# Kernel optimization log

Measured on AMD Instinct MI355X. Metric: run time of the kernel, lower is better.

## Reference

```python
import jax, jax.numpy as jnp
import numpy as np

N_NODES = 468  # MediaPipe face-mesh landmark count


def build_edges(n):
    # static edge structure from create_face_graph: i <-> j for j in i+1..min(i+10, n)
    src, dst = [], []
    for i in range(n):
        for j in range(i + 1, min(i + 10, n)):
            src += [i, j]
            dst += [j, i]
    # PyG GCNConv adds self-loops before normalization
    src = np.asarray(src + list(range(n)), dtype=np.int32)
    dst = np.asarray(dst + list(range(n)), dtype=np.int32)
    deg = np.bincount(dst, minlength=n).astype(np.float32)
    dinv = 1.0 / np.sqrt(deg)
    norm = (dinv[src] * dinv[dst]).astype(np.float32)
    return jnp.asarray(src), jnp.asarray(dst), jnp.asarray(norm)


def gcn_conv(x, W, b, src, dst, norm):
    # x: [B, N, d_in] -> [B, N, d_out]; GCNConv: transform then normalized scatter-add
    h = x @ W                                   # [B, N, d_out]
    msg = h[:, src, :] * norm[None, :, None]    # gather along node dim: [B, E, d_out]
    agg = jnp.zeros_like(h).at[:, dst, :].add(msg)
    return agg + b


def setup_inputs() -> dict:
    key = jax.random.key(0)
    ks = jax.random.split(key, 13)
    s = 0.05
    inp = {
        'landmarks': jax.random.normal(ks[0], (128, N_NODES * 3), dtype=jnp.float32),
        'W_enc': jax.random.normal(ks[1], (3, 64), dtype=jnp.float32) * s,
        'b_enc': jnp.zeros((64,), dtype=jnp.float32),
        'W1': jax.random.normal(ks[2], (64, 128), dtype=jnp.float32) * s,
        'b1': jnp.zeros((128,), dtype=jnp.float32),
        'W2': jax.random.normal(ks[3], (128, 256), dtype=jnp.float32) * s,
        'b2': jnp.zeros((256,), dtype=jnp.float32),
        'W3': jax.random.normal(ks[4], (256, 128), dtype=jnp.float32) * s,
        'b3': jnp.zeros((128,), dtype=jnp.float32),
        'W_fus': jax.random.normal(ks[5], (128, 512), dtype=jnp.float32) * s,
        'b_fus': jnp.zeros((512,), dtype=jnp.float32),
        'W_cls': jax.random.normal(ks[6], (512, 2), dtype=jnp.float32) * s,
        'b_cls': jnp.zeros((2,), dtype=jnp.float32),
    }
    return inp


def reference(landmarks, W_enc, b_enc, W1, b1, W2, b2, W3, b3, W_fus, b_fus, W_cls, b_cls):
    B = landmarks.shape[0]
    n = landmarks.shape[1] // 3
    src, dst, norm = build_edges(n)
    x = landmarks.reshape(B, n, 3) @ W_enc + b_enc            # node encoder [B,N,64]
    x = jax.nn.relu(gcn_conv(x, W1, b1, src, dst, norm))      # [B,N,128]
    x = jax.nn.relu(gcn_conv(x, W2, b2, src, dst, norm))      # [B,N,256]
    x = jax.nn.relu(gcn_conv(x, W3, b3, src, dst, norm))      # [B,N,128]
    graph_features = jnp.mean(x, axis=1)                      # global mean pool [B,128]
    features = jax.nn.relu(graph_features @ W_fus + b_fus)    # fusion (dropout=eval) [B,512]
    output = features @ W_cls + b_cls                         # classifier [B,2]
    return output, features, graph_features
```

## Files before the change

kernel.cpp:

```cpp
#include <hip/hip_runtime.h>
#include <hip/hip_bf16.h>

typedef __bf16 bf16x8 __attribute__((ext_vector_type(8)));
typedef float  f32x4  __attribute__((ext_vector_type(4)));
typedef unsigned short ushort_t;

#define NN 468

#define W1H 0
#define W1L 8192
#define W2H 16384
#define W2L 49152
#define W3H 81920
#define W3L 114688

#define L_X0   0
#define L_X1   0
#define L_X2   0
#define R1     43296
#define L_DTAB 76064
#define L_POOL 76544

#define MFMA3(d, ah, al, wh, wl)                                        \
    d = __builtin_amdgcn_mfma_f32_16x16x32_bf16(ah, wh, d, 0, 0, 0);    \
    d = __builtin_amdgcn_mfma_f32_16x16x32_bf16(ah, wl, d, 0, 0, 0);    \
    d = __builtin_amdgcn_mfma_f32_16x16x32_bf16(al, wh, d, 0, 0, 0);

__device__ __forceinline__ void pack_split4(const float* y,
                                            ushort_t* hdst, ushort_t* ldst) {
    ushort_t h[4], l[4];
    #pragma unroll
    for (int j = 0; j < 4; ++j) {
        __hip_bfloat16 hb = __float2bfloat16(y[j]);
        float hf = __bfloat162float(hb);
        __hip_bfloat16 lb = __float2bfloat16(y[j] - hf);
        h[j] = *(ushort_t*)&hb; l[j] = *(ushort_t*)&lb;
    }
    uint2 hv = make_uint2((unsigned)h[0] | ((unsigned)h[1] << 16),
                          (unsigned)h[2] | ((unsigned)h[3] << 16));
    uint2 lv = make_uint2((unsigned)l[0] | ((unsigned)l[1] << 16),
                          (unsigned)l[2] | ((unsigned)l[3] << 16));
    *(uint2*)hdst = hv;
    *(uint2*)ldst = lv;
}

__device__ __forceinline__ int frag_off(int r, int k, int K16) {
    return (r >> 4) * K16 + (k >> 5) * 512 + ((k >> 3) & 3) * 128
         + (r & 15) * 8 + (k & 7);
}

__device__ __forceinline__ int ywoff(int r, int k4, int K16) {
    int q = (k4 >> 3) & 3;
    int u = q * 16 + (((r & 15) ^ (q << 1)) & 15);
    return (r >> 4) * K16 + (k4 >> 5) * 512 + u * 8 + (k4 & 7);
}

__global__ __launch_bounds__(512, 4) void fused(
    const float* __restrict__ Lm, const ushort_t* __restrict__ wext,
    const float* __restrict__ We, const float* __restrict__ be,
    const float* __restrict__ b1, const float* __restrict__ b2,
    const float* __restrict__ b3, float* __restrict__ partial)
{
    __shared__ __align__(16) char lds[77056];
    float*    X0   = (float*)(lds + L_X0);
    float*    X1   = (float*)(lds + L_X1);
    float*    X2   = (float*)(lds + L_X2);
    float*    lmst = (float*)(lds + R1);
    ushort_t* Y1h  = (ushort_t*)(lds + R1);  ushort_t* Y1l = Y1h + 7168;
    ushort_t* Y2h  = (ushort_t*)(lds + R1);  ushort_t* Y2l = Y2h + 6144;
    ushort_t* Y3h  = (ushort_t*)(lds + R1);  ushort_t* Y3l = Y3h + 8192;
    float*    dtab = (float*)(lds + L_DTAB);
    float*    pool = (float*)(lds + L_POOL);

    const int tid  = threadIdx.x;
    const int lane = tid & 63;
    const int wave = tid >> 6;
    const int wm = wave & 1, wn = wave >> 1;
    const int l15 = lane & 15, lg = lane >> 4;
    const int lswz = (lane & 48) + (((lane & 15) ^ ((lane >> 4) << 1)) & 15);
    const int rt = blockIdx.x, b = blockIdx.y;
    const int r0 = rt * 64;

    if (tid < 118) {
        int ri = r0 - 27 + tid;
        float dv = 0.f;
        if (ri >= 0 && ri < NN) {
            int lo = ri - 9; if (lo < 0) lo = 0;
            int hi = ri + 9; if (hi > NN - 1) hi = NN - 1;
            dv = 1.0f / sqrtf((float)(hi - lo + 1));
        }
        dtab[tid] = dv;
    }
    if (tid < 354) {
        int g = (r0 - 27) * 3 + tid;
        lmst[tid] = (g >= 0 && g < NN * 3) ? Lm[(size_t)b * (NN * 3) + g] : 0.f;
    }
    if (tid < 128) pool[tid] = 0.f;
    __syncthreads();

    {
        const int c = tid & 63;
        const float w0 = We[c], w1 = We[64 + c], w2 = We[128 + c], bk = be[c];
        for (int l0 = tid >> 6; l0 < 118; l0 += 8) {
            float x = bk + lmst[l0*3]*w0 + lmst[l0*3+1]*w1 + lmst[l0*3+2]*w2;
            X0[l0 * 68 + c] = x * dtab[l0];
        }
    }
    __syncthreads();

    {
        const int c4 = (tid & 15) << 2;
        const int base = (tid >> 4) * 4;
        if (base < 100) {
            f32x4 ws = {};
            #pragma unroll
            for (int d = 0; d < 19; ++d)
                ws += *(const f32x4*)(X0 + (base + d) * 68 + c4);
            #pragma unroll
            for (int rr = 0; rr < 4; ++rr) {
                int row = base + rr;
                if (rr) ws += *(const f32x4*)(X0 + (row + 18) * 68 + c4)
                            - *(const f32x4*)(X0 + (row - 1)  * 68 + c4);
                float dv = dtab[row + 9];
                float y4[4] = {ws[0]*dv, ws[1]*dv, ws[2]*dv, ws[3]*dv};
                int off = ywoff(row, c4, 1024);
                pack_split4(y4, Y1h + off, Y1l + off);
            }
        } else if (base < 112) {
            float z4[4] = {0.f, 0.f, 0.f, 0.f};
            #pragma unroll
            for (int rr = 0; rr < 4; ++rr) {
                int row = base + rr;
                if (row < 112) {
                    int off = ywoff(row, c4, 1024);
                    pack_split4(z4, Y1h + off, Y1l + off);
                }
            }
        }
    }
    __syncthreads();

    f32x4 acc1[4][2] = {};
    __builtin_amdgcn_s_setprio(1);
    #pragma unroll
    for (int kt = 0; kt < 2; ++kt) {
        bf16x8 a[4][2];
        #pragma unroll
        for (int mt = 0; mt < 4; ++mt) {
            int t = wm*4 + mt; if (t > 6) t = 6;
            int off = t * 1024 + kt * 512 + lswz * 8;
            a[mt][0] = *(const bf16x8*)(Y1h + off);
            a[mt][1] = *(const bf16x8*)(Y1l + off);
        }
        #pragma unroll
        for (int nt = 0; nt < 2; ++nt) {
            int woff = (nt*4 + wn) * 1024 + kt * 512 + lane * 8;
            bf16x8 wh = *(const bf16x8*)(wext + W1H + woff);
            bf16x8 wl = *(const bf16x8*)(wext + W1L + woff);
            #pragma unroll
            for (int mt = 0; mt < 4; ++mt) {
                MFMA3(acc1[mt][nt], a[mt][0], a[mt][1], wh, wl);
            }
        }
    }
    __builtin_amdgcn_s_setprio(0);

    f32x4 acc2[3][4] = {};
    #pragma unroll
    for (int kc = 0; kc < 2; ++kc) {
        if (kc == 1) {
            __builtin_amdgcn_s_setprio(1);
            #pragma unroll
            for (int kt = 0; kt < 2; ++kt) {
                bf16x8 a[3][2];
                #pragma unroll
                for (int mt = 0; mt < 3; ++mt) {
                    int off = (wm*3 + mt) * 1024 + kt * 512 + lswz * 8;
                    a[mt][0] = *(const bf16x8*)(Y2h + off);
                    a[mt][1] = *(const bf16x8*)(Y2l + off);
                }
                #pragma unroll
                for (int nt = 0; nt < 4; ++nt) {
                    int woff = (nt*4 + wn) * 2048 + (0*2 + kt) * 512 + lane * 8;
                    bf16x8 wh = *(const bf16x8*)(wext + W2H + woff);
                    bf16x8 wl = *(const bf16x8*)(wext + W2L + woff);
                    #pragma unroll
                    for (int mt = 0; mt < 3; ++mt) {
                        MFMA3(acc2[mt][nt], a[mt][0], a[mt][1], wh, wl);
                    }
                }
            }
            __builtin_amdgcn_s_setprio(0);
        }
        #pragma unroll
        for (int mt = 0; mt < 4; ++mt) {
            int t = wm*4 + mt; if (t > 6) t = 6;
            int gcol = (kc*4 + wn)*16 + l15;
            int cl   = wn*16 + l15;
            float bv = b1[gcol];
            #pragma unroll
            for (int r = 0; r < 4; ++r) {
                int lr1 = t*16 + lg*4 + r;
                if (lr1 < 100)
                    X1[lr1*68 + cl] =
                        dtab[lr1 + 9] * fmaxf(acc1[mt][kc][r] + bv, 0.f);
            }
        }
        __syncthreads();

        {
            const int c4   = (tid & 15) << 2;
            const int base = (tid >> 4) * 3;
            f32x4 ws = {};
            if (base < 82) {
                #pragma unroll
                for (int d = 0; d < 19; ++d)
                    ws += *(const f32x4*)(X1 + (base + d) * 68 + c4);
            }
            #pragma unroll
            for (int rr = 0; rr < 3; ++rr) {
                int row = base + rr;
                if (row < 96) {
                    float y4[4] = {0.f, 0.f, 0.f, 0.f};
                    if (row < 82) {
                        if (rr) ws += *(const f32x4*)(X1 + (row + 18) * 68 + c4)
                                    - *(const f32x4*)(X1 + (row - 1)  * 68 + c4);
                        float dv = dtab[row + 18];
                        y4[0] = ws[0]*dv; y4[1] = ws[1]*dv;
                        y4[2] = ws[2]*dv; y4[3] = ws[3]*dv;
                    }
                    int off = ywoff(row, c4, 1024);
                    pack_split4(y4, Y2h + off, Y2l + off);
                }
            }
        }
        __syncthreads();
    }

    __builtin_amdgcn_s_setprio(1);
    #pragma unroll
    for (int kt = 0; kt < 2; ++kt) {
        bf16x8 a[3][2];
        #pragma unroll
        for (int mt = 0; mt < 3; ++mt) {
            int off = (wm*3 + mt) * 1024 + kt * 512 + lswz * 8;
            a[mt][0] = *(const bf16x8*)(Y2h + off);
            a[mt][1] = *(const bf16x8*)(Y2l + off);
        }
        #pragma unroll
        for (int nt = 0; nt < 4; ++nt) {
            int woff = (nt*4 + wn) * 2048 + (1*2 + kt) * 512 + lane * 8;
            bf16x8 wh = *(const bf16x8*)(wext + W2H + woff);
            bf16x8 wl = *(const bf16x8*)(wext + W2L + woff);
            #pragma unroll
            for (int mt = 0; mt < 3; ++mt) {
                MFMA3(acc2[mt][nt], a[mt][0], a[mt][1], wh, wl);
            }
        }
    }
    __builtin_amdgcn_s_setprio(0);

    f32x4 acc3[2][2] = {};
    #pragma unroll
    for (int nc = 0; nc < 2; ++nc) {
        if (nc == 1) {
            __builtin_amdgcn_s_setprio(1);
            #pragma unroll
            for (int kt = 0; kt < 4; ++kt) {
                bf16x8 a0[2], a1[2];
                #pragma unroll
                for (int mt = 0; mt < 2; ++mt) {
                    int aoff = (wm*2 + mt) * 2048 + kt * 512 + lswz * 8;
                    a0[mt] = *(const bf16x8*)(Y3h + aoff);
                    a1[mt] = *(const bf16x8*)(Y3l + aoff);
                }
                #pragma unroll
                for (int nt = 0; nt < 2; ++nt) {
                    int woff = (nt*4 + wn) * 4096 + (0*4 + kt) * 512 + lane * 8;
                    bf16x8 wh = *(const bf16x8*)(wext + W3H + woff);
                    bf16x8 wl = *(const bf16x8*)(wext + W3L + woff);
                    #pragma unroll
                    for (int mt = 0; mt < 2; ++mt) {
                        MFMA3(acc3[mt][nt], a0[mt], a1[mt], wh, wl);
                    }
                }
            }
            __builtin_amdgcn_s_setprio(0);
        }
        #pragma unroll
        for (int mt = 0; mt < 3; ++mt)
        #pragma unroll
        for (int q = 0; q < 2; ++q) {
            int gcol = ((nc*2 + q)*4 + wn)*16 + l15;
            int cl   = (q*4 + wn)*16 + l15;
            float bv = b2[gcol];
            #pragma unroll
            for (int r = 0; r < 4; ++r) {
                int lr2 = (wm*3 + mt)*16 + lg*4 + r;
                if (lr2 < 82)
                    X2[lr2*132 + cl] =
                        dtab[lr2 + 18] * fmaxf(acc2[mt][nc*2 + q][r] + bv, 0.f);
            }
        }
        __syncthreads();

        {
            const int c4   = (tid & 31) << 2;
            const int base = (tid >> 5) * 4;
            f32x4 ws = {};
            #pragma unroll
            for (int d = 0; d < 19; ++d)
                ws += *(const f32x4*)(X2 + (base + d) * 132 + c4);
            #pragma unroll
            for (int rr = 0; rr < 4; ++rr) {
                int row = base + rr;
                if (rr) ws += *(const f32x4*)(X2 + (row + 18) * 132 + c4)
                            - *(const f32x4*)(X2 + (row - 1)  * 132 + c4);
                float dv = dtab[row + 27];
                float y4[4] = {ws[0]*dv, ws[1]*dv, ws[2]*dv, ws[3]*dv};
                int off = ywoff(row, c4, 2048);
                pack_split4(y4, Y3h + off, Y3l + off);
            }
        }
        __syncthreads();
    }

    __builtin_amdgcn_s_setprio(1);
    #pragma unroll
    for (int kt = 0; kt < 4; ++kt) {
        bf16x8 a0[2], a1[2];
        #pragma unroll
        for (int mt = 0; mt < 2; ++mt) {
            int aoff = (wm*2 + mt) * 2048 + kt * 512 + lswz * 8;
            a0[mt] = *(const bf16x8*)(Y3h + aoff);
            a1[mt] = *(const bf16x8*)(Y3l + aoff);
        }
        #pragma unroll
        for (int nt = 0; nt < 2; ++nt) {
            int woff = (nt*4 + wn) * 4096 + (1*4 + kt) * 512 + lane * 8;
            bf16x8 wh = *(const bf16x8*)(wext + W3H + woff);
            bf16x8 wl = *(const bf16x8*)(wext + W3L + woff);
            #pragma unroll
            for (int mt = 0; mt < 2; ++mt) {
                MFMA3(acc3[mt][nt], a0[mt], a1[mt], wh, wl);
            }
        }
    }
    __builtin_amdgcn_s_setprio(0);

    #pragma unroll
    for (int nt = 0; nt < 2; ++nt) {
        int g_t = nt*4 + wn;
        float bv = b3[g_t*16 + l15];
        float cs = 0.f;
        #pragma unroll
        for (int mt = 0; mt < 2; ++mt)
        #pragma unroll
        for (int r = 0; r < 4; ++r) {
            int gr = r0 + (wm*2 + mt)*16 + lg*4 + r;
            if (gr < NN) cs += fmaxf(acc3[mt][nt][r] + bv, 0.f);
        }
        cs += __shfl_xor(cs, 16);
        cs += __shfl_xor(cs, 32);
        if (lane < 16) atomicAdd(&pool[g_t*16 + lane], cs);
    }
    __syncthreads();
    if (tid < 128) partial[((size_t)b * 8 + rt) * 128 + tid] = pool[tid];
}

__global__ __launch_bounds__(256) void wconv(
    const float* __restrict__ W1, const float* __restrict__ W2,
    const float* __restrict__ W3, ushort_t* __restrict__ wext)
{
    int i = blockIdx.x * 256 + threadIdx.x;
    float w; int off_h, off_l, idx;
    if (i < 8192) {
        int k = i >> 7, n = i & 127;
        w = W1[i]; idx = frag_off(n, k, 1024);  off_h = W1H; off_l = W1L;
    } else if (i < 40960) {
        int j = i - 8192;
        int k = j >> 8, n = j & 255;
        w = W2[j]; idx = frag_off(n, k, 2048);  off_h = W2H; off_l = W2L;
    } else if (i < 73728) {
        int j = i - 40960;
        int k = j >> 7, n = j & 127;
        w = W3[j]; idx = frag_off(n, k, 4096);  off_h = W3H; off_l = W3L;
    } else return;
    __hip_bfloat16 hb = __float2bfloat16(w);
    float hf = __bfloat162float(hb);
    __hip_bfloat16 lb = __float2bfloat16(w - hf);
    wext[off_h + idx] = *(ushort_t*)&hb;
    wext[off_l + idx] = *(ushort_t*)&lb;
}

__global__ __launch_bounds__(512) void head_kernel(
    const float* __restrict__ partial, const float* __restrict__ Wf,
    const float* __restrict__ bf, const float* __restrict__ Wc,
    const float* __restrict__ bc, float* __restrict__ dout)
{
    __shared__ float gfs[128];
    __shared__ float feats[512];
    int b = blockIdx.x, t = threadIdx.x;
    if (t < 128) {
        const float* p = partial + (size_t)b * (8 * 128);
        float s = 0.f;
        #pragma unroll
        for (int tt = 0; tt < 8; ++tt) s += p[tt * 128 + t];
        s *= (1.0f / 468.0f);
        gfs[t] = s;
        dout[65792 + b * 128 + t] = s;
    }
    __syncthreads();
    float a = bf[t];
    for (int k = 0; k < 128; ++k) a += gfs[k] * Wf[k * 512 + t];
    a = fmaxf(a, 0.f);
    dout[256 + b * 512 + t] = a;
    feats[t] = a;
    __syncthreads();
    if (t < 64) {
        float s0 = 0.f, s1 = 0.f;
        for (int c = t; c < 512; c += 64) {
            float f = feats[c];
            s0 += f * Wc[c * 2 + 0];
            s1 += f * Wc[c * 2 + 1];
        }
        #pragma unroll
        for (int off = 32; off; off >>= 1) {
            s0 += __shfl_down(s0, off);
            s1 += __shfl_down(s1, off);
        }
        if (t == 0) {
            dout[b * 2 + 0] = s0 + bc[0];
            dout[b * 2 + 1] = s1 + bc[1];
        }
    }
}

extern "C" void kernel_launch(void* const* d_in, const int* in_sizes, int n_in,
                              void* d_out, int out_size, void* d_ws, size_t ws_size,
                              hipStream_t stream)
{
    const float* landmarks = (const float*)d_in[0];
    const float* W_enc     = (const float*)d_in[1];
    const float* b_enc     = (const float*)d_in[2];
    const float* W1        = (const float*)d_in[3];
    const float* b1        = (const float*)d_in[4];
    const float* W2        = (const float*)d_in[5];
    const float* b2        = (const float*)d_in[6];
    const float* W3        = (const float*)d_in[7];
    const float* b3        = (const float*)d_in[8];
    const float* W_fus     = (const float*)d_in[9];
    const float* b_fus     = (const float*)d_in[10];
    const float* W_cls     = (const float*)d_in[11];
    const float* b_cls     = (const float*)d_in[12];
    float* out = (float*)d_out;

    char* ws = (char*)d_ws;
    ushort_t* wext = (ushort_t*)(ws + 0);
    float* partial = (float*)(ws + 294912);

    wconv<<<288, 256, 0, stream>>>(W1, W2, W3, wext);
    fused<<<dim3(8, 128), 512, 0, stream>>>(
        landmarks, wext, W_enc, b_enc, b1, b2, b3, partial);
    head_kernel<<<128, 512, 0, stream>>>(partial, W_fus, b_fus, W_cls, b_cls, out);
}
```

Measured before the change: 69.59 us.

## Store full Y2 in separate LDS region and run layer-2 GEMM after both chunks

Gives the layer-2 aggregated input Y2 a full 128-column buffer at its own LDS offset instead of reusing one half-size region per column chunk. The two K-chunks of the layer-2 GEMM, previously interleaved with the aggregation passes, now run as one 4-step K loop after both chunks are written. LDS is re-laid out with new offsets and grows slightly, and a barrier is added before layer 3. This lowers register pressure during aggregation and gives one longer MFMA loop, but loses the overlap of chunk-0 MFMAs with chunk-1 aggregation and may reduce occupancy.

```diff
diff --git a/kernel.cpp b/kernel.cpp
--- a/kernel.cpp
+++ b/kernel.cpp
@@ -14,12 +14,12 @@
 #define W3H 81920
 #define W3L 114688
 
-#define L_X0   0
-#define L_X1   0
-#define L_X2   0
-#define R1     43296
-#define L_DTAB 76064
-#define L_POOL 76544
+#define L_Y1   32096
+#define L_Y2   27200
+#define L_Y3   43296
+#define L_LM   76352
+#define L_DTAB 77768
+#define L_POOL 78240
 
 #define MFMA3(d, ah, al, wh, wl)                                        \
     d = __builtin_amdgcn_mfma_f32_16x16x32_bf16(ah, wh, d, 0, 0, 0);    \
@@ -61,14 +61,12 @@
     const float* __restrict__ b1, const float* __restrict__ b2,
     const float* __restrict__ b3, float* __restrict__ partial)
 {
-    __shared__ __align__(16) char lds[77056];
-    float*    X0   = (float*)(lds + L_X0);
-    float*    X1   = (float*)(lds + L_X1);
-    float*    X2   = (float*)(lds + L_X2);
-    float*    lmst = (float*)(lds + R1);
-    ushort_t* Y1h  = (ushort_t*)(lds + R1);  ushort_t* Y1l = Y1h + 7168;
-    ushort_t* Y2h  = (ushort_t*)(lds + R1);  ushort_t* Y2l = Y2h + 6144;
-    ushort_t* Y3h  = (ushort_t*)(lds + R1);  ushort_t* Y3l = Y3h + 8192;
+    __shared__ __align__(16) char lds[78752];
+    float*    X    = (float*)(lds);
+    ushort_t* Y1h  = (ushort_t*)(lds + L_Y1);  ushort_t* Y1l = Y1h + 7168;
+    ushort_t* Y2h  = (ushort_t*)(lds + L_Y2);  ushort_t* Y2l = Y2h + 12288;
+    ushort_t* Y3h  = (ushort_t*)(lds + L_Y3);  ushort_t* Y3l = Y3h + 8192;
+    float*    lmst = (float*)(lds + L_LM);
     float*    dtab = (float*)(lds + L_DTAB);
     float*    pool = (float*)(lds + L_POOL);
 
@@ -103,7 +101,7 @@
         const float w0 = We[c], w1 = We[64 + c], w2 = We[128 + c], bk = be[c];
         for (int l0 = tid >> 6; l0 < 118; l0 += 8) {
             float x = bk + lmst[l0*3]*w0 + lmst[l0*3+1]*w1 + lmst[l0*3+2]*w2;
-            X0[l0 * 68 + c] = x * dtab[l0];
+            X[l0 * 68 + c] = x * dtab[l0];
         }
     }
     __syncthreads();
@@ -115,12 +113,12 @@
             f32x4 ws = {};
             #pragma unroll
             for (int d = 0; d < 19; ++d)
-                ws += *(const f32x4*)(X0 + (base + d) * 68 + c4);
+                ws += *(const f32x4*)(X + (base + d) * 68 + c4);
             #pragma unroll
             for (int rr = 0; rr < 4; ++rr) {
                 int row = base + rr;
-                if (rr) ws += *(const f32x4*)(X0 + (row + 18) * 68 + c4)
-                            - *(const f32x4*)(X0 + (row - 1)  * 68 + c4);
+                if (rr) ws += *(const f32x4*)(X + (row + 18) * 68 + c4)
+                            - *(const f32x4*)(X + (row - 1)  * 68 + c4);
                 float dv = dtab[row + 9];
                 float y4[4] = {ws[0]*dv, ws[1]*dv, ws[2]*dv, ws[3]*dv};
                 int off = ywoff(row, c4, 1024);
@@ -165,33 +163,8 @@
     }
     __builtin_amdgcn_s_setprio(0);
 
-    f32x4 acc2[3][4] = {};
     #pragma unroll
     for (int kc = 0; kc < 2; ++kc) {
-        if (kc == 1) {
-            __builtin_amdgcn_s_setprio(1);
-            #pragma unroll
-            for (int kt = 0; kt < 2; ++kt) {
-                bf16x8 a[3][2];
-                #pragma unroll
-                for (int mt = 0; mt < 3; ++mt) {
-                    int off = (wm*3 + mt) * 1024 + kt * 512 + lswz * 8;
-                    a[mt][0] = *(const bf16x8*)(Y2h + off);
-                    a[mt][1] = *(const bf16x8*)(Y2l + off);
-                }
-                #pragma unroll
-                for (int nt = 0; nt < 4; ++nt) {
-                    int woff = (nt*4 + wn) * 2048 + (0*2 + kt) * 512 + lane * 8;
-                    bf16x8 wh = *(const bf16x8*)(wext + W2H + woff);
-                    bf16x8 wl = *(const bf16x8*)(wext + W2L + woff);
-                    #pragma unroll
-                    for (int mt = 0; mt < 3; ++mt) {
-                        MFMA3(acc2[mt][nt], a[mt][0], a[mt][1], wh, wl);
-                    }
-                }
-            }
-            __builtin_amdgcn_s_setprio(0);
-        }
         #pragma unroll
         for (int mt = 0; mt < 4; ++mt) {
             int t = wm*4 + mt; if (t > 6) t = 6;
@@ -202,7 +175,7 @@
             for (int r = 0; r < 4; ++r) {
                 int lr1 = t*16 + lg*4 + r;
                 if (lr1 < 100)
-                    X1[lr1*68 + cl] =
+                    X[lr1*68 + cl] =
                         dtab[lr1 + 9] * fmaxf(acc1[mt][kc][r] + bv, 0.f);
             }
         }
@@ -215,7 +188,7 @@
             if (base < 82) {
                 #pragma unroll
                 for (int d = 0; d < 19; ++d)
-                    ws += *(const f32x4*)(X1 + (base + d) * 68 + c4);
+                    ws += *(const f32x4*)(X + (base + d) * 68 + c4);
             }
             #pragma unroll
             for (int rr = 0; rr < 3; ++rr) {
@@ -223,13 +196,13 @@
                 if (row < 96) {
                     float y4[4] = {0.f, 0.f, 0.f, 0.f};
                     if (row < 82) {
-                        if (rr) ws += *(const f32x4*)(X1 + (row + 18) * 68 + c4)
-                                    - *(const f32x4*)(X1 + (row - 1)  * 68 + c4);
+                        if (rr) ws += *(const f32x4*)(X + (row + 18) * 68 + c4)
+                                    - *(const f32x4*)(X + (row - 1)  * 68 + c4);
                         float dv = dtab[row + 18];
                         y4[0] = ws[0]*dv; y4[1] = ws[1]*dv;
                         y4[2] = ws[2]*dv; y4[3] = ws[3]*dv;
                     }
-                    int off = ywoff(row, c4, 1024);
+                    int off = ywoff(row, kc*64 + c4, 2048);
                     pack_split4(y4, Y2h + off, Y2l + off);
                 }
             }
@@ -237,19 +210,20 @@
         __syncthreads();
     }
 
+    f32x4 acc2[3][4] = {};
     __builtin_amdgcn_s_setprio(1);
     #pragma unroll
-    for (int kt = 0; kt < 2; ++kt) {
+    for (int kt = 0; kt < 4; ++kt) {
         bf16x8 a[3][2];
         #pragma unroll
         for (int mt = 0; mt < 3; ++mt) {
-            int off = (wm*3 + mt) * 1024 + kt * 512 + lswz * 8;
+            int off = (wm*3 + mt) * 2048 + kt * 512 + lswz * 8;
             a[mt][0] = *(const bf16x8*)(Y2h + off);
             a[mt][1] = *(const bf16x8*)(Y2l + off);
         }
         #pragma unroll
         for (int nt = 0; nt < 4; ++nt) {
-            int woff = (nt*4 + wn) * 2048 + (1*2 + kt) * 512 + lane * 8;
+            int woff = (nt*4 + wn) * 2048 + kt * 512 + lane * 8;
             bf16x8 wh = *(const bf16x8*)(wext + W2H + woff);
             bf16x8 wl = *(const bf16x8*)(wext + W2L + woff);
             #pragma unroll
@@ -259,6 +233,7 @@
         }
     }
     __builtin_amdgcn_s_setprio(0);
+    __syncthreads();
 
     f32x4 acc3[2][2] = {};
     #pragma unroll
@@ -298,7 +273,7 @@
             for (int r = 0; r < 4; ++r) {
                 int lr2 = (wm*3 + mt)*16 + lg*4 + r;
                 if (lr2 < 82)
-                    X2[lr2*132 + cl] =
+                    X[lr2*132 + cl] =
                         dtab[lr2 + 18] * fmaxf(acc2[mt][nc*2 + q][r] + bv, 0.f);
             }
         }
@@ -310,12 +285,12 @@
             f32x4 ws = {};
             #pragma unroll
             for (int d = 0; d < 19; ++d)
-                ws += *(const f32x4*)(X2 + (base + d) * 132 + c4);
+                ws += *(const f32x4*)(X + (base + d) * 132 + c4);
             #pragma unroll
             for (int rr = 0; rr < 4; ++rr) {
                 int row = base + rr;
-                if (rr) ws += *(const f32x4*)(X2 + (row + 18) * 132 + c4)
-                            - *(const f32x4*)(X2 + (row - 1)  * 132 + c4);
+                if (rr) ws += *(const f32x4*)(X + (row + 18) * 132 + c4)
+                            - *(const f32x4*)(X + (row - 1)  * 132 + c4);
                 float dv = dtab[row + 27];
                 float y4[4] = {ws[0]*dv, ws[1]*dv, ws[2]*dv, ws[3]*dv};
                 int off = ywoff(row, c4, 2048);
```

After: 66.79 us, median of 2. -4.0%, faster.
